# Kernel optimization log

Hardware: AMD Instinct MI355X
Metric: run time of the kernel (lower is better)

Reference implementation:

```python
import jax, jax.numpy as jnp
import numpy as np

N = 100000      # nodes
E = 1600000     # edges (avg degree 16)
F_IN = 128      # num_features
H = 64          # hidden_dim
C = 7           # num_classes


def setup_inputs() -> dict:
    key = jax.random.key(0)
    ks = jax.random.split(key, 9)
    x = jax.random.normal(ks[0], (N, F_IN), dtype=jnp.float32)
    edge_index = jax.random.randint(ks[1], (2, E), 0, N, dtype=jnp.int32)
    s1 = 1.0 / np.sqrt(F_IN)
    s2 = 1.0 / np.sqrt(H)
    # SAGEConv1: lin_l applied to aggregated neighbors, lin_r to root
    W1l = jax.random.uniform(ks[2], (F_IN, H), jnp.float32, -s1, s1)
    W1r = jax.random.uniform(ks[3], (F_IN, H), jnp.float32, -s1, s1)
    b1 = jax.random.uniform(ks[4], (H,), jnp.float32, -s1, s1)
    # SAGEConv2
    W2l = jax.random.uniform(ks[5], (H, C), jnp.float32, -s2, s2)
    W2r = jax.random.uniform(ks[6], (H, C), jnp.float32, -s2, s2)
    b2 = jax.random.uniform(ks[7], (C,), jnp.float32, -s2, s2)
    return {"x": x, "edge_index": edge_index, "W1l": W1l, "W1r": W1r,
            "b1": b1, "W2l": W2l, "W2r": W2r, "b2": b2}


def _segment_mean(vals, idx, num_segments):
    # scatter-mean: sum messages per destination node, divide by in-degree
    sums = jax.ops.segment_sum(vals, idx, num_segments=num_segments)
    cnt = jax.ops.segment_sum(jnp.ones(idx.shape, vals.dtype), idx,
                              num_segments=num_segments)
    return sums / jnp.maximum(cnt, 1.0)[:, None]


def reference(x, edge_index, W1l, W1r, b1, W2l, W2r, b2):
    src, dst = edge_index[0], edge_index[1]
    # SAGEConv 1: mean of neighbor (src) features at each dst, plus root term
    agg1 = _segment_mean(x[src], dst, N)              # [N, F_IN]
    h = agg1 @ W1l + x @ W1r + b1                     # [N, H]
    h = jax.nn.relu(h)
    # dropout is inactive in eval mode (deterministic reference)
    # SAGEConv 2
    agg2 = _segment_mean(h[src], dst, N)              # [N, H]
    out = agg2 @ W2l + h @ W2r + b2                   # [N, C]
    return jax.nn.log_softmax(out, axis=1)
```

## Files before the change

kernel.cpp:

```cpp
#include <hip/hip_runtime.h>
#include <cstdint>
#include <cstddef>


#define CAP 64
#define BINSZ 128
#define CH 4096

typedef __attribute__((ext_vector_type(8))) short bf16x8v;
typedef __attribute__((ext_vector_type(4))) float f32x4v;

__device__ __forceinline__ float bf2f(unsigned short u) {
  return __uint_as_float(((unsigned int)u) << 16);
}
__device__ __forceinline__ unsigned short f2bf(float f) {
  unsigned int x = __float_as_uint(f);
  unsigned int r = (x + 0x7fffu + ((x >> 16) & 1u)) >> 16;
  return (unsigned short)r;
}

__global__ __launch_bounds__(256) void k_hist(const int* __restrict__ ei,
                                              int* __restrict__ hist,
                                              const float* __restrict__ W1l,
                                              const float* __restrict__ W1r,
                                              unsigned short* __restrict__ wswz,
                                              int E, int NB, int NCH) {
  const int t = threadIdx.x;
  if (blockIdx.x >= (unsigned)NCH) {
    int idx = (blockIdx.x - NCH) * 256 + t;
    int j = idx & 7;
    int lane = (idx >> 3) & 63;
    int c = (idx >> 9) & 7;
    int t4 = idx >> 12;
    int kk = t4 * 32 + (lane >> 4) * 8 + j;
    int nn = c * 16 + (lane & 15);
    float v = (nn < 64) ? W1l[kk * 64 + nn] : W1r[kk * 64 + (nn - 64)];
    wswz[idx] = f2bf(v);
    return;
  }
  __shared__ int lcnt[1024];
  const int c = blockIdx.x;
  for (int i = t; i < NB; i += 256) lcnt[i] = 0;
  __syncthreads();
  const int base = c * CH;
  const int end = min(base + CH, E);
  for (int e = base + t; e < end; e += 256) {
    int d = ei[E + e];
    atomicAdd(&lcnt[d >> 7], 1);
  }
  __syncthreads();
  for (int i = t; i < NB; i += 256) hist[(size_t)i * NCH + c] = lcnt[i];
}

__global__ __launch_bounds__(256) void k_scan_gemm(
    int* __restrict__ hist, int* __restrict__ tot, int NB, int NCH, int nScan,
    const float* __restrict__ x, const unsigned short* __restrict__ wswz,
    const float* __restrict__ b1, unsigned short* __restrict__ xl,
    unsigned short* __restrict__ hroot, int Nn) {
  if (blockIdx.x < (unsigned)nScan) {
    const int lane = threadIdx.x & 63;
    const int bin = blockIdx.x * 4 + (threadIdx.x >> 6);
    if (bin >= NB) return;
    int* h = hist + (size_t)bin * NCH;
    int carry = 0;
    for (int base = 0; base < NCH; base += 64) {
      int i = base + lane;
      int v = (i < NCH) ? h[i] : 0;
      int incl = v;
      #pragma unroll
      for (int d = 1; d < 64; d <<= 1) {
        int t = __shfl_up(incl, d, 64);
        if (lane >= d) incl += t;
      }
      if (i < NCH) h[i] = carry + incl - v;
      carry += __shfl(incl, 63, 64);
    }
    if (lane == 0) tot[bin] = carry;
    return;
  }
  __shared__ unsigned short Bsw[16384];
  const int t = threadIdx.x;
  const int bid = blockIdx.x - nScan;
  {
    const uint4* src = (const uint4*)wswz;
    uint4* dst = (uint4*)Bsw;
    #pragma unroll
    for (int i = 0; i < 8; ++i) dst[t + i * 256] = src[t + i * 256];
  }
  __syncthreads();

  const int lane = t & 63;
  const int wid = t >> 6;
  const int quad = lane >> 4;
  const int m = lane & 15;
  const int rowA = bid * 64 + wid * 16 + m;
  const float* xrow = x + (size_t)min(rowA, Nn - 1) * 128;

  f32x4v acc[8];
  #pragma unroll
  for (int c = 0; c < 8; ++c) acc[c] = (f32x4v){0.f, 0.f, 0.f, 0.f};

  #pragma unroll
  for (int t4 = 0; t4 < 4; ++t4) {
    const int koff = t4 * 32 + quad * 8;
    float4 a0 = *(const float4*)(xrow + koff);
    float4 a1 = *(const float4*)(xrow + koff + 4);
    bf16x8v af;
    af[0] = (short)f2bf(a0.x); af[1] = (short)f2bf(a0.y);
    af[2] = (short)f2bf(a0.z); af[3] = (short)f2bf(a0.w);
    af[4] = (short)f2bf(a1.x); af[5] = (short)f2bf(a1.y);
    af[6] = (short)f2bf(a1.z); af[7] = (short)f2bf(a1.w);
    #pragma unroll
    for (int c = 0; c < 8; ++c) {
      const bf16x8v bf_ = *(const bf16x8v*)&Bsw[(((t4 * 8 + c) * 64 + lane)) << 3];
      acc[c] = __builtin_amdgcn_mfma_f32_16x16x32_bf16(af, bf_, acc[c], 0, 0, 0);
    }
  }

  const int rbase = bid * 64 + wid * 16 + quad * 4;
  #pragma unroll
  for (int c = 0; c < 8; ++c) {
    const int col = c * 16 + m;
    #pragma unroll
    for (int i = 0; i < 4; ++i) {
      const int r = rbase + i;
      if (r < Nn) {
        if (c < 4) xl[(size_t)r * 64 + col] = f2bf(acc[c][i]);
        else       hroot[(size_t)r * 64 + (col - 64)] = f2bf(acc[c][i] + b1[col - 64]);
      }
    }
  }
}

__global__ __launch_bounds__(64) void k_scanB(const int* __restrict__ tot,
                                              int* __restrict__ binbase, int NB) {
  const int lane = threadIdx.x;
  int carry = 0;
  for (int base = 0; base < NB; base += 64) {
    int i = base + lane;
    int v = (i < NB) ? tot[i] : 0;
    int incl = v;
    #pragma unroll
    for (int d = 1; d < 64; d <<= 1) {
      int t = __shfl_up(incl, d, 64);
      if (lane >= d) incl += t;
    }
    if (i < NB) binbase[i] = carry + incl - v;
    carry += __shfl(incl, 63, 64);
  }
  if (lane == 0) binbase[NB] = carry;
}

__global__ __launch_bounds__(256) void k_scat(const int* __restrict__ ei,
                                              const int* __restrict__ hist,
                                              const int* __restrict__ binbase,
                                              unsigned int* __restrict__ part,
                                              int E, int NB, int NCH) {
  __shared__ int lcur[1024];
  const int c = blockIdx.x, t = threadIdx.x;
  for (int i = t; i < NB; i += 256)
    lcur[i] = hist[(size_t)i * NCH + c] + binbase[i];
  __syncthreads();
  const int base = c * CH;
  const int end = min(base + CH, E);
  for (int e = base + t; e < end; e += 256) {
    int s = ei[e];
    int d = ei[E + e];
    int bin = d >> 7;
    int pos = atomicAdd(&lcur[bin], 1);
    part[pos] = (unsigned)s | ((unsigned)(d & 127) << 17);
  }
}

__global__ __launch_bounds__(256) void k_bucketB(const int* __restrict__ binbase,
                                                 const unsigned int* __restrict__ part,
                                                 int* __restrict__ cnt,
                                                 int* __restrict__ bucket) {
  __shared__ int lbkt[BINSZ * CAP];
  __shared__ int ldeg[BINSZ];
  const int b = blockIdx.x, t = threadIdx.x;
  if (t < BINSZ) ldeg[t] = 0;
  __syncthreads();
  const int e0 = binbase[b], e1 = binbase[b + 1];
  for (int i = e0 + t; i < e1; i += 256) {
    unsigned rec = part[i];
    int loc = rec >> 17;
    int p = atomicAdd(&ldeg[loc], 1);
    if (p < CAP) lbkt[loc * CAP + p] = (int)(rec & 0x1FFFFu);
  }
  __syncthreads();
  if (t < BINSZ) cnt[b * BINSZ + t] = ldeg[t];
  const int4* s4 = (const int4*)lbkt;
  int4* d4 = (int4*)(bucket + (size_t)b * BINSZ * CAP);
  #pragma unroll 2
  for (int i = t; i < BINSZ * CAP / 4; i += 256) d4[i] = s4[i];
}

__global__ __launch_bounds__(256) void k_agg1(
    const int* __restrict__ cnt, const int* __restrict__ bucket,
    const unsigned int* __restrict__ xl32, const unsigned int* __restrict__ hroot32,
    unsigned int* __restrict__ hbuf32, int Nn) {
  const int lane = threadIdx.x & 63;
  const int q = lane & 15;
  const int g = lane >> 4;
  const int nw = gridDim.x * (blockDim.x >> 6);
  int n = blockIdx.x * (blockDim.x >> 6) + (threadIdx.x >> 6);
  if (n >= Nn) return;

  int c  = cnt[n];
  int c1 = cnt[min(n + nw, Nn - 1)];
  int m = c < CAP ? c : CAP;
  int sidx = (lane < m) ? bucket[(size_t)n * CAP + lane] : 0;
  if ((unsigned)sidx >= (unsigned)Nn) sidx = 0;
  uint2 hu = *(const uint2*)(hroot32 + (size_t)n * 32 + 2 * q);

  while (true) {
    const int n1 = n + nw;
    const int n1c = min(n1, Nn - 1);
    const int m1 = c1 < CAP ? c1 : CAP;
    int sidx1 = (lane < m1) ? bucket[(size_t)n1c * CAP + lane] : 0;
    uint2 hu1 = *(const uint2*)(hroot32 + (size_t)n1c * 32 + 2 * q);
    int c2 = cnt[min(n1 + nw, Nn - 1)];

    float a0 = 0.f, a1 = 0.f, a2 = 0.f, a3 = 0.f;
    int i = 0;
    for (; i + 16 <= m; i += 16) {
      int rA = __shfl(sidx, i + g, 64);
      int rB = __shfl(sidx, i + 4 + g, 64);
      int rC = __shfl(sidx, i + 8 + g, 64);
      int rD = __shfl(sidx, i + 12 + g, 64);
      uint2 uA = *(const uint2*)(xl32 + (size_t)rA * 32 + 2 * q);
      uint2 uB = *(const uint2*)(xl32 + (size_t)rB * 32 + 2 * q);
      uint2 uC = *(const uint2*)(xl32 + (size_t)rC * 32 + 2 * q);
      uint2 uD = *(const uint2*)(xl32 + (size_t)rD * 32 + 2 * q);
      a0 += (__uint_as_float(uA.x << 16) + __uint_as_float(uB.x << 16))
          + (__uint_as_float(uC.x << 16) + __uint_as_float(uD.x << 16));
      a1 += (__uint_as_float(uA.x & 0xFFFF0000u) + __uint_as_float(uB.x & 0xFFFF0000u))
          + (__uint_as_float(uC.x & 0xFFFF0000u) + __uint_as_float(uD.x & 0xFFFF0000u));
      a2 += (__uint_as_float(uA.y << 16) + __uint_as_float(uB.y << 16))
          + (__uint_as_float(uC.y << 16) + __uint_as_float(uD.y << 16));
      a3 += (__uint_as_float(uA.y & 0xFFFF0000u) + __uint_as_float(uB.y & 0xFFFF0000u))
          + (__uint_as_float(uC.y & 0xFFFF0000u) + __uint_as_float(uD.y & 0xFFFF0000u));
    }
    for (; i + 8 <= m; i += 8) {
      int rA = __shfl(sidx, i + g, 64);
      int rB = __shfl(sidx, i + 4 + g, 64);
      uint2 uA = *(const uint2*)(xl32 + (size_t)rA * 32 + 2 * q);
      uint2 uB = *(const uint2*)(xl32 + (size_t)rB * 32 + 2 * q);
      a0 += __uint_as_float(uA.x << 16) + __uint_as_float(uB.x << 16);
      a1 += __uint_as_float(uA.x & 0xFFFF0000u) + __uint_as_float(uB.x & 0xFFFF0000u);
      a2 += __uint_as_float(uA.y << 16) + __uint_as_float(uB.y << 16);
      a3 += __uint_as_float(uA.y & 0xFFFF0000u) + __uint_as_float(uB.y & 0xFFFF0000u);
    }
    for (; i < m; i += 4) {
      int e = i + g;
      int r = __shfl(sidx, e & 63, 64);
      uint2 u = *(const uint2*)(xl32 + (size_t)r * 32 + 2 * q);
      if (e < m) {
        a0 += __uint_as_float(u.x << 16);
        a1 += __uint_as_float(u.x & 0xFFFF0000u);
        a2 += __uint_as_float(u.y << 16);
        a3 += __uint_as_float(u.y & 0xFFFF0000u);
      }
    }
    a0 += __shfl_xor(a0, 16, 64); a0 += __shfl_xor(a0, 32, 64);
    a1 += __shfl_xor(a1, 16, 64); a1 += __shfl_xor(a1, 32, 64);
    a2 += __shfl_xor(a2, 16, 64); a2 += __shfl_xor(a2, 32, 64);
    a3 += __shfl_xor(a3, 16, 64); a3 += __shfl_xor(a3, 32, 64);
    if (g == 0) {
      float dd = c > 0 ? (float)c : 1.f;
      float h0 = fmaxf(a0 / dd + __uint_as_float(hu.x << 16), 0.f);
      float h1 = fmaxf(a1 / dd + __uint_as_float(hu.x & 0xFFFF0000u), 0.f);
      float h2 = fmaxf(a2 / dd + __uint_as_float(hu.y << 16), 0.f);
      float h3 = fmaxf(a3 / dd + __uint_as_float(hu.y & 0xFFFF0000u), 0.f);
      uint2 o;
      o.x = (unsigned)f2bf(h0) | ((unsigned)f2bf(h1) << 16);
      o.y = (unsigned)f2bf(h2) | ((unsigned)f2bf(h3) << 16);
      *(uint2*)(hbuf32 + (size_t)n * 32 + 2 * q) = o;
    }
    if (n1 >= Nn) break;
    n = n1; c = c1; c1 = c2; m = m1;
    sidx = ((unsigned)sidx1 >= (unsigned)Nn) ? 0 : sidx1;
    hu = hu1;
  }
}

__global__ __launch_bounds__(128) void k_gemm2(
    const unsigned short* __restrict__ hbuf,
    const float* __restrict__ W2l, const float* __restrict__ W2r,
    const float* __restrict__ b2,
    float* __restrict__ hl, float* __restrict__ hr, int Nn) {
  __shared__ float tile[128 * 65];
  const int t = threadIdx.x;
  const int rowbase = blockIdx.x * 128;
  for (int idx = t; idx < 128 * 64; idx += 128) {
    int r = idx >> 6, k = idx & 63;
    int n = rowbase + r;
    tile[r * 65 + k] = (n < Nn) ? bf2f(hbuf[(size_t)n * 64 + k]) : 0.f;
  }
  __syncthreads();
  int n = rowbase + t;
  if (n >= Nn) return;
  float al[7] = {0, 0, 0, 0, 0, 0, 0};
  float ar[7] = {0, 0, 0, 0, 0, 0, 0};
  for (int k = 0; k < 64; ++k) {
    float hv = tile[t * 65 + k];
    #pragma unroll
    for (int c = 0; c < 7; ++c) {
      al[c] = fmaf(hv, W2l[k * 7 + c], al[c]);
      ar[c] = fmaf(hv, W2r[k * 7 + c], ar[c]);
    }
  }
  #pragma unroll
  for (int c = 0; c < 7; ++c) {
    hl[(size_t)n * 8 + c] = al[c];
    hr[(size_t)n * 8 + c] = ar[c] + b2[c];
  }
  hl[(size_t)n * 8 + 7] = 0.f;
  hr[(size_t)n * 8 + 7] = 0.f;
}

__global__ __launch_bounds__(256) void k_out(
    const int* __restrict__ cnt, const int* __restrict__ bucket,
    const float* __restrict__ hl, const float* __restrict__ hr,
    float* __restrict__ out, int Nn) {
  const int lane = threadIdx.x & 63;
  const int c = lane & 7;
  const int sub = lane >> 3;
  const int gw = blockIdx.x * (blockDim.x >> 6) + (threadIdx.x >> 6);
  const int n = gw * 8 + sub;
  if (n >= Nn) return;
  int cn = cnt[n];
  int m = cn < CAP ? cn : CAP;
  const bool act = (c < 7);
  float acc = 0.f;
  for (int e0 = 0; e0 < m; e0 += 8) {
    int bv = (e0 + c < m) ? bucket[(size_t)n * CAP + e0 + c] : 0;
    #pragma unroll
    for (int cc = 0; cc < 8; ++cc) {
      if (e0 + cc < m) {
        int s = __shfl(bv, (lane & 56) + cc, 64);
        if ((unsigned)s >= (unsigned)Nn) s = 0;
        if (act) acc += hl[(size_t)s * 8 + c];
      }
    }
  }
  float dd = cn > 0 ? (float)cn : 1.f;
  float v = act ? (acc / dd + hr[(size_t)n * 8 + c]) : -INFINITY;
  float mx = v;
  mx = fmaxf(mx, __shfl_xor(mx, 1, 8));
  mx = fmaxf(mx, __shfl_xor(mx, 2, 8));
  mx = fmaxf(mx, __shfl_xor(mx, 4, 8));
  float ex = act ? expf(v - mx) : 0.f;
  float s2 = ex;
  s2 += __shfl_xor(s2, 1, 8);
  s2 += __shfl_xor(s2, 2, 8);
  s2 += __shfl_xor(s2, 4, 8);
  float res = v - mx - logf(s2);
  if (act) out[(size_t)n * 7 + c] = res;
}

static inline size_t alignup(size_t v) { return (v + 255) & ~(size_t)255; }

extern "C" void kernel_launch(void* const* d_in, const int* in_sizes, int n_in,
                              void* d_out, int out_size, void* d_ws, size_t ws_size,
                              hipStream_t stream) {
  const int N = in_sizes[0] / 128;
  const int E = in_sizes[1] / 2;
  const int NB = (N + BINSZ - 1) / BINSZ;
  const int Np = NB * BINSZ;
  const int NCH = (E + CH - 1) / CH;
  const int nScan = (NB + 3) / 4;

  const float* x   = (const float*)d_in[0];
  const int*   ei  = (const int*)d_in[1];
  const float* W1l = (const float*)d_in[2];
  const float* W1r = (const float*)d_in[3];
  const float* b1  = (const float*)d_in[4];
  const float* W2l = (const float*)d_in[5];
  const float* W2r = (const float*)d_in[6];
  const float* b2  = (const float*)d_in[7];
  float* out = (float*)d_out;

  char* p = (char*)d_ws;
  int* hist    = (int*)p;            p += alignup((size_t)NB * NCH * 4);
  int* tot     = (int*)p;            p += alignup((size_t)NB * 4);
  int* binbase = (int*)p;            p += alignup((size_t)(NB + 1) * 4);
  unsigned int* part = (unsigned int*)p; p += alignup((size_t)E * 4);
  int* cnt    = (int*)p;             p += alignup((size_t)Np * 4);
  int* bucket = (int*)p;             p += alignup((size_t)Np * CAP * 4);
  unsigned short* wswz = (unsigned short*)p; p += alignup((size_t)16384 * 2);
  unsigned short* xl    = (unsigned short*)p; p += alignup((size_t)N * 64 * 2);
  unsigned short* hroot = (unsigned short*)p; p += alignup((size_t)N * 64 * 2);
  unsigned short* hbuf  = (unsigned short*)p; p += alignup((size_t)N * 64 * 2);
  float* hl  = (float*)p;            p += alignup((size_t)N * 8 * 4);
  float* hr  = (float*)p;            p += alignup((size_t)N * 8 * 4);

  dim3 b256(256);
  k_hist<<<dim3(NCH + 64), b256, 0, stream>>>(ei, hist, W1l, W1r, wswz, E, NB, NCH);
  k_scan_gemm<<<dim3(nScan + (N + 63) / 64), b256, 0, stream>>>(
      hist, tot, NB, NCH, nScan, x, wswz, b1, xl, hroot, N);
  k_scanB<<<dim3(1), dim3(64), 0, stream>>>(tot, binbase, NB);
  k_scat<<<dim3(NCH), b256, 0, stream>>>(ei, hist, binbase, part, E, NB, NCH);
  k_bucketB<<<dim3(NB), b256, 0, stream>>>(binbase, part, cnt, bucket);
  k_agg1<<<dim3(2048), b256, 0, stream>>>(cnt, bucket,
      (const unsigned int*)xl, (const unsigned int*)hroot, (unsigned int*)hbuf, N);
  k_gemm2<<<dim3((N + 127) / 128), dim3(128), 0, stream>>>(hbuf, W2l, W2r, b2, hl, hr, N);
  const int waves_out = (N + 7) / 8;
  k_out<<<dim3((waves_out + 3) / 4), b256, 0, stream>>>(cnt, bucket, hl, hr, out, N);
}
```

Baseline: 241.9 us.

## Drop scanB via atomic bin allocation, use fp32 intermediates, two-node agg1 interleave

Bin base offsets are now assigned with an atomic cursor inside the scan blocks instead of a separate single-wave scan kernel. This removes one launch, but the bins are no longer laid out in order, so bucketB takes each bin's extent from tot. The xl, hroot and hbuf intermediates move from bf16 to fp32, which removes pack and unpack work but doubles the gather traffic in agg1. agg1 now handles two nodes per wave at a time to expose more memory-level parallelism.

```diff
diff --git a/kernel.cpp b/kernel.cpp
--- a/kernel.cpp
+++ b/kernel.cpp
@@ -24,9 +24,11 @@
                                               const float* __restrict__ W1l,
                                               const float* __restrict__ W1r,
                                               unsigned short* __restrict__ wswz,
+                                              int* __restrict__ cursor,
                                               int E, int NB, int NCH) {
   const int t = threadIdx.x;
   if (blockIdx.x >= (unsigned)NCH) {
+    if (blockIdx.x == (unsigned)NCH && t == 0) *cursor = 0;
     int idx = (blockIdx.x - NCH) * 256 + t;
     int j = idx & 7;
     int lane = (idx >> 3) & 63;
@@ -53,10 +55,11 @@
 }
 
 __global__ __launch_bounds__(256) void k_scan_gemm(
-    int* __restrict__ hist, int* __restrict__ tot, int NB, int NCH, int nScan,
+    int* __restrict__ hist, int* __restrict__ tot, int* __restrict__ binbase,
+    int* __restrict__ cursor, int NB, int NCH, int nScan,
     const float* __restrict__ x, const unsigned short* __restrict__ wswz,
-    const float* __restrict__ b1, unsigned short* __restrict__ xl,
-    unsigned short* __restrict__ hroot, int Nn) {
+    const float* __restrict__ b1, float* __restrict__ xl,
+    float* __restrict__ hroot, int Nn) {
   if (blockIdx.x < (unsigned)nScan) {
     const int lane = threadIdx.x & 63;
     const int bin = blockIdx.x * 4 + (threadIdx.x >> 6);
@@ -75,7 +78,10 @@
       if (i < NCH) h[i] = carry + incl - v;
       carry += __shfl(incl, 63, 64);
     }
-    if (lane == 0) tot[bin] = carry;
+    if (lane == 0) {
+      tot[bin] = carry;
+      binbase[bin] = atomicAdd(cursor, carry);
+    }
     return;
   }
   __shared__ unsigned short Bsw[16384];
@@ -125,30 +131,11 @@
     for (int i = 0; i < 4; ++i) {
       const int r = rbase + i;
       if (r < Nn) {
-        if (c < 4) xl[(size_t)r * 64 + col] = f2bf(acc[c][i]);
-        else       hroot[(size_t)r * 64 + (col - 64)] = f2bf(acc[c][i] + b1[col - 64]);
+        if (c < 4) xl[(size_t)r * 64 + col] = acc[c][i];
+        else       hroot[(size_t)r * 64 + (col - 64)] = acc[c][i] + b1[col - 64];
       }
     }
   }
-}
-
-__global__ __launch_bounds__(64) void k_scanB(const int* __restrict__ tot,
-                                              int* __restrict__ binbase, int NB) {
-  const int lane = threadIdx.x;
-  int carry = 0;
-  for (int base = 0; base < NB; base += 64) {
-    int i = base + lane;
-    int v = (i < NB) ? tot[i] : 0;
-    int incl = v;
-    #pragma unroll
-    for (int d = 1; d < 64; d <<= 1) {
-      int t = __shfl_up(incl, d, 64);
-      if (lane >= d) incl += t;
-    }
-    if (i < NB) binbase[i] = carry + incl - v;
-    carry += __shfl(incl, 63, 64);
-  }
-  if (lane == 0) binbase[NB] = carry;
 }
 
 __global__ __launch_bounds__(256) void k_scat(const int* __restrict__ ei,
@@ -173,6 +160,7 @@
 }
 
 __global__ __launch_bounds__(256) void k_bucketB(const int* __restrict__ binbase,
+                                                 const int* __restrict__ tot,
                                                  const unsigned int* __restrict__ part,
                                                  int* __restrict__ cnt,
                                                  int* __restrict__ bucket) {
@@ -181,7 +169,7 @@
   const int b = blockIdx.x, t = threadIdx.x;
   if (t < BINSZ) ldeg[t] = 0;
   __syncthreads();
-  const int e0 = binbase[b], e1 = binbase[b + 1];
+  const int e0 = binbase[b], e1 = e0 + tot[b];
   for (int i = e0 + t; i < e1; i += 256) {
     unsigned rec = part[i];
     int loc = rec >> 17;
@@ -196,97 +184,163 @@
   for (int i = t; i < BINSZ * CAP / 4; i += 256) d4[i] = s4[i];
 }
 
+#define GLOAD4(sidx, i, u0, u1, u2, u3)                          \
+  {                                                              \
+    int r0_ = __shfl(sidx, (i) + g, 64);                         \
+    int r1_ = __shfl(sidx, (i) + 4 + g, 64);                     \
+    int r2_ = __shfl(sidx, (i) + 8 + g, 64);                     \
+    int r3_ = __shfl(sidx, (i) + 12 + g, 64);                    \
+    u0 = *(const float4*)(xlf + (size_t)r0_ * 64 + 4 * q);       \
+    u1 = *(const float4*)(xlf + (size_t)r1_ * 64 + 4 * q);       \
+    u2 = *(const float4*)(xlf + (size_t)r2_ * 64 + 4 * q);       \
+    u3 = *(const float4*)(xlf + (size_t)r3_ * 64 + 4 * q);       \
+  }
+#define GACC4(u0, u1, u2, u3, a0, a1, a2, a3)                    \
+  {                                                              \
+    a0 += (u0.x + u1.x) + (u2.x + u3.x);                         \
+    a1 += (u0.y + u1.y) + (u2.y + u3.y);                         \
+    a2 += (u0.z + u1.z) + (u2.z + u3.z);                         \
+    a3 += (u0.w + u1.w) + (u2.w + u3.w);                         \
+  }
+#define GLOAD2(sidx, i, u0, u1)                                  \
+  {                                                              \
+    int r0_ = __shfl(sidx, (i) + g, 64);                         \
+    int r1_ = __shfl(sidx, (i) + 4 + g, 64);                     \
+    u0 = *(const float4*)(xlf + (size_t)r0_ * 64 + 4 * q);       \
+    u1 = *(const float4*)(xlf + (size_t)r1_ * 64 + 4 * q);       \
+  }
+#define GACC2(u0, u1, a0, a1, a2, a3)                            \
+  {                                                              \
+    a0 += u0.x + u1.x; a1 += u0.y + u1.y;                        \
+    a2 += u0.z + u1.z; a3 += u0.w + u1.w;                        \
+  }
+#define GTAIL(sidx, ii, mm, a0, a1, a2, a3)                      \
+  {                                                              \
+    int e_ = (ii) + g;                                           \
+    int r_ = __shfl(sidx, e_ & 63, 64);                          \
+    float4 u_ = *(const float4*)(xlf + (size_t)r_ * 64 + 4 * q); \
+    if (e_ < (mm)) { a0 += u_.x; a1 += u_.y; a2 += u_.z; a3 += u_.w; } \
+  }
+
 __global__ __launch_bounds__(256) void k_agg1(
     const int* __restrict__ cnt, const int* __restrict__ bucket,
-    const unsigned int* __restrict__ xl32, const unsigned int* __restrict__ hroot32,
-    unsigned int* __restrict__ hbuf32, int Nn) {
+    const float* __restrict__ xlf, const float* __restrict__ hrootf,
+    float* __restrict__ hbuff, int Nn) {
   const int lane = threadIdx.x & 63;
   const int q = lane & 15;
   const int g = lane >> 4;
   const int nw = gridDim.x * (blockDim.x >> 6);
-  int n = blockIdx.x * (blockDim.x >> 6) + (threadIdx.x >> 6);
-  if (n >= Nn) return;
-
-  int c  = cnt[n];
-  int c1 = cnt[min(n + nw, Nn - 1)];
-  int m = c < CAP ? c : CAP;
-  int sidx = (lane < m) ? bucket[(size_t)n * CAP + lane] : 0;
-  if ((unsigned)sidx >= (unsigned)Nn) sidx = 0;
-  uint2 hu = *(const uint2*)(hroot32 + (size_t)n * 32 + 2 * q);
+  const int stride = nw << 1;
+  int nA = blockIdx.x * (blockDim.x >> 6) + (threadIdx.x >> 6);
+  if (nA >= Nn) return;
+
+  int nB = nA + nw;
+  int nBc = min(nB, Nn - 1);
+  int cA = cnt[nA];
+  int cB = cnt[nBc];
+  int rA0 = bucket[(size_t)nA * CAP + lane];
+  int rB0 = bucket[(size_t)nBc * CAP + lane];
+  int mA = cA < CAP ? cA : CAP;
+  int mB = cB < CAP ? cB : CAP;
+  int sidxA = (lane < mA && (unsigned)rA0 < (unsigned)Nn) ? rA0 : 0;
+  int sidxB = (lane < mB && (unsigned)rB0 < (unsigned)Nn) ? rB0 : 0;
 
   while (true) {
-    const int n1 = n + nw;
-    const int n1c = min(n1, Nn - 1);
-    const int m1 = c1 < CAP ? c1 : CAP;
-    int sidx1 = (lane < m1) ? bucket[(size_t)n1c * CAP + lane] : 0;
-    uint2 hu1 = *(const uint2*)(hroot32 + (size_t)n1c * 32 + 2 * q);
-    int c2 = cnt[min(n1 + nw, Nn - 1)];
-
-    float a0 = 0.f, a1 = 0.f, a2 = 0.f, a3 = 0.f;
-    int i = 0;
-    for (; i + 16 <= m; i += 16) {
-      int rA = __shfl(sidx, i + g, 64);
-      int rB = __shfl(sidx, i + 4 + g, 64);
-      int rC = __shfl(sidx, i + 8 + g, 64);
-      int rD = __shfl(sidx, i + 12 + g, 64);
-      uint2 uA = *(const uint2*)(xl32 + (size_t)rA * 32 + 2 * q);
-      uint2 uB = *(const uint2*)(xl32 + (size_t)rB * 32 + 2 * q);
-      uint2 uC = *(const uint2*)(xl32 + (size_t)rC * 32 + 2 * q);
-      uint2 uD = *(const uint2*)(xl32 + (size_t)rD * 32 + 2 * q);
-      a0 += (__uint_as_float(uA.x << 16) + __uint_as_float(uB.x << 16))
-          + (__uint_as_float(uC.x << 16) + __uint_as_float(uD.x << 16));
-      a1 += (__uint_as_float(uA.x & 0xFFFF0000u) + __uint_as_float(uB.x & 0xFFFF0000u))
-          + (__uint_as_float(uC.x & 0xFFFF0000u) + __uint_as_float(uD.x & 0xFFFF0000u));
-      a2 += (__uint_as_float(uA.y << 16) + __uint_as_float(uB.y << 16))
-          + (__uint_as_float(uC.y << 16) + __uint_as_float(uD.y << 16));
-      a3 += (__uint_as_float(uA.y & 0xFFFF0000u) + __uint_as_float(uB.y & 0xFFFF0000u))
-          + (__uint_as_float(uC.y & 0xFFFF0000u) + __uint_as_float(uD.y & 0xFFFF0000u));
-    }
-    for (; i + 8 <= m; i += 8) {
-      int rA = __shfl(sidx, i + g, 64);
-      int rB = __shfl(sidx, i + 4 + g, 64);
-      uint2 uA = *(const uint2*)(xl32 + (size_t)rA * 32 + 2 * q);
-      uint2 uB = *(const uint2*)(xl32 + (size_t)rB * 32 + 2 * q);
-      a0 += __uint_as_float(uA.x << 16) + __uint_as_float(uB.x << 16);
-      a1 += __uint_as_float(uA.x & 0xFFFF0000u) + __uint_as_float(uB.x & 0xFFFF0000u);
-      a2 += __uint_as_float(uA.y << 16) + __uint_as_float(uB.y << 16);
-      a3 += __uint_as_float(uA.y & 0xFFFF0000u) + __uint_as_float(uB.y & 0xFFFF0000u);
-    }
-    for (; i < m; i += 4) {
-      int e = i + g;
-      int r = __shfl(sidx, e & 63, 64);
-      uint2 u = *(const uint2*)(xl32 + (size_t)r * 32 + 2 * q);
-      if (e < m) {
-        a0 += __uint_as_float(u.x << 16);
-        a1 += __uint_as_float(u.x & 0xFFFF0000u);
-        a2 += __uint_as_float(u.y << 16);
-        a3 += __uint_as_float(u.y & 0xFFFF0000u);
+    const int nA1 = nA + stride;
+    const int nA1c = min(nA1, Nn - 1);
+    const int nB1c = min(nA1 + nw, Nn - 1);
+    int cA1 = cnt[nA1c];
+    int cB1 = cnt[nB1c];
+    int rawA1 = bucket[(size_t)nA1c * CAP + lane];
+    int rawB1 = bucket[(size_t)nB1c * CAP + lane];
+    float4 huA = *(const float4*)(hrootf + (size_t)nA * 64 + 4 * q);
+    float4 huB = *(const float4*)(hrootf + (size_t)nBc * 64 + 4 * q);
+
+    float aA0 = 0.f, aA1 = 0.f, aA2 = 0.f, aA3 = 0.f;
+    float aB0 = 0.f, aB1 = 0.f, aB2 = 0.f, aB3 = 0.f;
+    int iA = 0, iB = 0;
+    while (iA + 16 <= mA && iB + 16 <= mB) {
+      float4 A0, A1, A2, A3, B0, B1, B2, B3;
+      GLOAD4(sidxA, iA, A0, A1, A2, A3);
+      GLOAD4(sidxB, iB, B0, B1, B2, B3);
+      GACC4(A0, A1, A2, A3, aA0, aA1, aA2, aA3);
+      GACC4(B0, B1, B2, B3, aB0, aB1, aB2, aB3);
+      iA += 16; iB += 16;
+    }
+    while (iA + 16 <= mA) {
+      float4 A0, A1, A2, A3;
+      GLOAD4(sidxA, iA, A0, A1, A2, A3);
+      GACC4(A0, A1, A2, A3, aA0, aA1, aA2, aA3);
+      iA += 16;
+    }
+    while (iB + 16 <= mB) {
+      float4 B0, B1, B2, B3;
+      GLOAD4(sidxB, iB, B0, B1, B2, B3);
+      GACC4(B0, B1, B2, B3, aB0, aB1, aB2, aB3);
+      iB += 16;
+    }
+    {
+      const bool e8A = (iA + 8 <= mA), e8B = (iB + 8 <= mB);
+      if (e8A && e8B) {
+        float4 A0, A1, B0, B1;
+        GLOAD2(sidxA, iA, A0, A1);
+        GLOAD2(sidxB, iB, B0, B1);
+        GACC2(A0, A1, aA0, aA1, aA2, aA3);
+        GACC2(B0, B1, aB0, aB1, aB2, aB3);
+        iA += 8; iB += 8;
+      } else if (e8A) {
+        float4 A0, A1;
+        GLOAD2(sidxA, iA, A0, A1);
+        GACC2(A0, A1, aA0, aA1, aA2, aA3);
+        iA += 8;
+      } else if (e8B) {
+        float4 B0, B1;
+        GLOAD2(sidxB, iB, B0, B1);
+        GACC2(B0, B1, aB0, aB1, aB2, aB3);
+        iB += 8;
       }
     }
-    a0 += __shfl_xor(a0, 16, 64); a0 += __shfl_xor(a0, 32, 64);
-    a1 += __shfl_xor(a1, 16, 64); a1 += __shfl_xor(a1, 32, 64);
-    a2 += __shfl_xor(a2, 16, 64); a2 += __shfl_xor(a2, 32, 64);
-    a3 += __shfl_xor(a3, 16, 64); a3 += __shfl_xor(a3, 32, 64);
+    for (; iA < mA; iA += 4) GTAIL(sidxA, iA, mA, aA0, aA1, aA2, aA3);
+    for (; iB < mB; iB += 4) GTAIL(sidxB, iB, mB, aB0, aB1, aB2, aB3);
+
+    aA0 += __shfl_xor(aA0, 16, 64); aA0 += __shfl_xor(aA0, 32, 64);
+    aA1 += __shfl_xor(aA1, 16, 64); aA1 += __shfl_xor(aA1, 32, 64);
+    aA2 += __shfl_xor(aA2, 16, 64); aA2 += __shfl_xor(aA2, 32, 64);
+    aA3 += __shfl_xor(aA3, 16, 64); aA3 += __shfl_xor(aA3, 32, 64);
+    aB0 += __shfl_xor(aB0, 16, 64); aB0 += __shfl_xor(aB0, 32, 64);
+    aB1 += __shfl_xor(aB1, 16, 64); aB1 += __shfl_xor(aB1, 32, 64);
+    aB2 += __shfl_xor(aB2, 16, 64); aB2 += __shfl_xor(aB2, 32, 64);
+    aB3 += __shfl_xor(aB3, 16, 64); aB3 += __shfl_xor(aB3, 32, 64);
     if (g == 0) {
-      float dd = c > 0 ? (float)c : 1.f;
-      float h0 = fmaxf(a0 / dd + __uint_as_float(hu.x << 16), 0.f);
-      float h1 = fmaxf(a1 / dd + __uint_as_float(hu.x & 0xFFFF0000u), 0.f);
-      float h2 = fmaxf(a2 / dd + __uint_as_float(hu.y << 16), 0.f);
-      float h3 = fmaxf(a3 / dd + __uint_as_float(hu.y & 0xFFFF0000u), 0.f);
-      uint2 o;
-      o.x = (unsigned)f2bf(h0) | ((unsigned)f2bf(h1) << 16);
-      o.y = (unsigned)f2bf(h2) | ((unsigned)f2bf(h3) << 16);
-      *(uint2*)(hbuf32 + (size_t)n * 32 + 2 * q) = o;
-    }
-    if (n1 >= Nn) break;
-    n = n1; c = c1; c1 = c2; m = m1;
-    sidx = ((unsigned)sidx1 >= (unsigned)Nn) ? 0 : sidx1;
-    hu = hu1;
+      float invA = 1.f / (cA > 0 ? (float)cA : 1.f);
+      float4 o;
+      o.x = fmaxf(fmaf(aA0, invA, huA.x), 0.f);
+      o.y = fmaxf(fmaf(aA1, invA, huA.y), 0.f);
+      o.z = fmaxf(fmaf(aA2, invA, huA.z), 0.f);
+      o.w = fmaxf(fmaf(aA3, invA, huA.w), 0.f);
+      *(float4*)(hbuff + (size_t)nA * 64 + 4 * q) = o;
+      if (nB < Nn) {
+        float invB = 1.f / (cB > 0 ? (float)cB : 1.f);
+        float4 p2;
+        p2.x = fmaxf(fmaf(aB0, invB, huB.x), 0.f);
+        p2.y = fmaxf(fmaf(aB1, invB, huB.y), 0.f);
+        p2.z = fmaxf(fmaf(aB2, invB, huB.z), 0.f);
+        p2.w = fmaxf(fmaf(aB3, invB, huB.w), 0.f);
+        *(float4*)(hbuff + (size_t)nB * 64 + 4 * q) = p2;
+      }
+    }
+    if (nA1 >= Nn) break;
+    nA = nA1; nB = nA + nw; nBc = min(nB, Nn - 1);
+    cA = cA1; cB = cB1;
+    mA = cA < CAP ? cA : CAP;
+    mB = cB < CAP ? cB : CAP;
+    sidxA = (lane < mA && (unsigned)rawA1 < (unsigned)Nn) ? rawA1 : 0;
+    sidxB = (lane < mB && (unsigned)rawB1 < (unsigned)Nn) ? rawB1 : 0;
   }
 }
 
 __global__ __launch_bounds__(128) void k_gemm2(
-    const unsigned short* __restrict__ hbuf,
+    const float* __restrict__ hbuf,
     const float* __restrict__ W2l, const float* __restrict__ W2r,
     const float* __restrict__ b2,
     float* __restrict__ hl, float* __restrict__ hr, int Nn) {
@@ -296,7 +350,7 @@
   for (int idx = t; idx < 128 * 64; idx += 128) {
     int r = idx >> 6, k = idx & 63;
     int n = rowbase + r;
-    tile[r * 65 + k] = (n < Nn) ? bf2f(hbuf[(size_t)n * 64 + k]) : 0.f;
+    tile[r * 65 + k] = (n < Nn) ? hbuf[(size_t)n * 64 + k] : 0.f;
   }
   __syncthreads();
   int n = rowbase + t;
@@ -386,25 +440,24 @@
   int* hist    = (int*)p;            p += alignup((size_t)NB * NCH * 4);
   int* tot     = (int*)p;            p += alignup((size_t)NB * 4);
   int* binbase = (int*)p;            p += alignup((size_t)(NB + 1) * 4);
+  int* cursor  = (int*)p;            p += alignup(4);
   unsigned int* part = (unsigned int*)p; p += alignup((size_t)E * 4);
   int* cnt    = (int*)p;             p += alignup((size_t)Np * 4);
   int* bucket = (int*)p;             p += alignup((size_t)Np * CAP * 4);
   unsigned short* wswz = (unsigned short*)p; p += alignup((size_t)16384 * 2);
-  unsigned short* xl    = (unsigned short*)p; p += alignup((size_t)N * 64 * 2);
-  unsigned short* hroot = (unsigned short*)p; p += alignup((size_t)N * 64 * 2);
-  unsigned short* hbuf  = (unsigned short*)p; p += alignup((size_t)N * 64 * 2);
+  float* xl    = (float*)p;          p += alignup((size_t)N * 64 * 4);
+  float* hroot = (float*)p;          p += alignup((size_t)N * 64 * 4);
+  float* hbuf  = (float*)p;          p += alignup((size_t)N * 64 * 4);
   float* hl  = (float*)p;            p += alignup((size_t)N * 8 * 4);
   float* hr  = (float*)p;            p += alignup((size_t)N * 8 * 4);
 
   dim3 b256(256);
-  k_hist<<<dim3(NCH + 64), b256, 0, stream>>>(ei, hist, W1l, W1r, wswz, E, NB, NCH);
+  k_hist<<<dim3(NCH + 64), b256, 0, stream>>>(ei, hist, W1l, W1r, wswz, cursor, E, NB, NCH);
   k_scan_gemm<<<dim3(nScan + (N + 63) / 64), b256, 0, stream>>>(
-      hist, tot, NB, NCH, nScan, x, wswz, b1, xl, hroot, N);
-  k_scanB<<<dim3(1), dim3(64), 0, stream>>>(tot, binbase, NB);
+      hist, tot, binbase, cursor, NB, NCH, nScan, x, wswz, b1, xl, hroot, N);
   k_scat<<<dim3(NCH), b256, 0, stream>>>(ei, hist, binbase, part, E, NB, NCH);
-  k_bucketB<<<dim3(NB), b256, 0, stream>>>(binbase, part, cnt, bucket);
-  k_agg1<<<dim3(2048), b256, 0, stream>>>(cnt, bucket,
-      (const unsigned int*)xl, (const unsigned int*)hroot, (unsigned int*)hbuf, N);
+  k_bucketB<<<dim3(NB), b256, 0, stream>>>(binbase, tot, part, cnt, bucket);
+  k_agg1<<<dim3(2048), b256, 0, stream>>>(cnt, bucket, xl, hroot, hbuf, N);
   k_gemm2<<<dim3((N + 127) / 128), dim3(128), 0, stream>>>(hbuf, W2l, W2r, b2, hl, hr, N);
   const int waves_out = (N + 7) / 8;
   k_out<<<dim3((waves_out + 3) / 4), b256, 0, stream>>>(cnt, bucket, hl, hr, out, N);
```

Result: slower. 284.6 us (+17.6%).
